# Performance work log

Measured on AMD Instinct MI355X. Metric: run time of the kernel, lower is better.

## Reference

```python
import jax, jax.numpy as jnp
import numpy as np

B, NNB, D, FF, L = 128, 510, 128, 512, 3
N = NNB + 2  # 2 query tokens (first/last) + neighbors
SQRT_D = float(np.sqrt(D))
LOGIT_CLIP = 10.0
NINF = -1e9


def _layer_norm(x, g, b):
    m = jnp.mean(x, axis=-1, keepdims=True)
    v = jnp.var(x, axis=-1, keepdims=True)
    return (x - m) * jax.lax.rsqrt(v + 1e-5) * g + b


def _aafm(q, k, v, w):
    # Attention-free module: sigmoid(q) * (exp(w) @ (exp(k)*v)) / (exp(w) @ exp(k))
    w = w - jnp.max(w, axis=-1, keepdims=True)          # stable, cancels in ratio
    k = k - jnp.max(k, axis=1, keepdims=True)
    ew = jnp.exp(w)                                      # [B,N,N]
    ek = jnp.exp(k)                                      # [B,N,D]
    num = jnp.einsum('bts,bsd->btd', ew, ek * v)
    den = jnp.einsum('bts,bsd->btd', ew, ek)
    return jax.nn.sigmoid(q) * num / den


def setup_inputs() -> dict:
    key = jax.random.key(0)
    ks = jax.random.split(key, 32)
    s = 1.0 / np.sqrt(D)
    inp = {
        'lower_xy': jax.random.uniform(ks[0], (B, N, 2), jnp.float32),
        'load': jax.random.uniform(ks[1], (B,), jnp.float32) * 0.9 + 0.1,
        'lower_demand': jax.random.uniform(ks[2], (B, NNB, 1), jnp.float32) * 0.3,
        'lower_cur_ninf_mask': jnp.where(
            jax.random.uniform(ks[3], (B, 1, N)) < 0.1, NINF, 0.0).astype(jnp.float32),
        'lower_pairwise_dist': jax.random.uniform(ks[4], (B, N, N), jnp.float32),
        'neighbors_num_list': jnp.full((B,), NNB, dtype=jnp.int32),
        'lower_neighbors_index': jax.random.randint(ks[5], (B, NNB), 0, 100000),
        # learned params (torch Linear stored transposed: here [in, out], y = x @ W)
        'emb_W': jax.random.normal(ks[6], (2, D)) * s,
        'emb_b': jnp.zeros((D,), jnp.float32),
        'w_load': jax.random.normal(ks[7], (D,)) * s,
        'w_demand': jax.random.normal(ks[8], (D,)) * s,
        'Wq_first': jax.random.normal(ks[9], (D, D)) * s,
        'Wq_last': jax.random.normal(ks[10], (D, D)) * s,
        'alpha_com': jnp.ones((1,), jnp.float32),
        'Wq': jax.random.normal(ks[11], (L, D, D)) * s,
        'Wk': jax.random.normal(ks[12], (L, D, D)) * s,
        'Wv': jax.random.normal(ks[13], (L, D, D)) * s,
        'alpha_attn': jnp.ones((L,), jnp.float32),
        'ln1_g': jnp.ones((L, D), jnp.float32),
        'ln1_b': jnp.zeros((L, D), jnp.float32),
        'ln2_g': jnp.ones((L, D), jnp.float32),
        'ln2_b': jnp.zeros((L, D), jnp.float32),
        'ff_W1': jax.random.normal(ks[14], (L, D, FF)) * s,
        'ff_b1': jnp.zeros((L, FF), jnp.float32),
        'ff_W2': jax.random.normal(ks[15], (L, FF, D)) * (1.0 / np.sqrt(FF)),
        'ff_b2': jnp.zeros((L, D), jnp.float32),
    }
    return inp


def reference(lower_xy, load, lower_demand, lower_cur_ninf_mask, lower_pairwise_dist,
              neighbors_num_list, lower_neighbors_index,
              emb_W, emb_b, w_load, w_demand, Wq_first, Wq_last, alpha_com,
              Wq, Wk, Wv, alpha_attn, ln1_g, ln1_b, ln2_g, ln2_b,
              ff_W1, ff_b1, ff_W2, ff_b2):
    load3 = load[:, None, None]                           # [B,1,1]
    load3 = jnp.where(load3 == 0, 1.0, load3)
    fln = lower_xy @ emb_W + emb_b                        # [B,N,D]
    load_emb = load3 * w_load                             # [B,1,D]
    q_first = fln[:, 0:1] @ Wq_first + load_emb
    q_last = fln[:, 1:2] @ Wq_last + load_emb
    demand = jnp.clip(lower_demand / load3, 0.0, 1.0)     # [B,n,1]
    nb = fln[:, 2:] + demand * w_demand                   # [B,n,D]
    nb_mask = lower_cur_ninf_mask[:, 0, 2:]               # [B,n]
    nb = jnp.where((nb_mask < 0)[..., None], 0.0, nb)     # padding overwrite
    x = jnp.concatenate([q_first, q_last, nb], axis=1)    # [B,N,D]

    log_nb = jnp.log2(neighbors_num_list.astype(x.dtype))[:, None, None]
    spd = -log_nb * lower_pairwise_dist                   # [B,N,N]
    mask_full = jnp.broadcast_to(lower_cur_ninf_mask, spd.shape)

    for i in range(L):
        q = x @ Wq[i]; k = x @ Wk[i]; v = x @ Wv[i]
        aafm = _aafm(q, k, v, alpha_attn[i] * spd + mask_full)
        h = _layer_norm(x + aafm, ln1_g[i], ln1_b[i])
        ff = jax.nn.relu(h @ ff_W1[i] + ff_b1[i]) @ ff_W2[i] + ff_b2[i]
        x = _layer_norm(h + ff, ln2_g[i], ln2_b[i])

    q_out = x[:, 0:1] + x[:, 1:2]                         # [B,1,D]
    nbo = x[:, 2:]                                        # [B,n,D]
    bias_com = alpha_com * spd[:, 1, 2:][:, None, :]      # [B,1,n]
    score = jnp.einsum('bqd,bnd->bqn', q_out, nbo) / SQRT_D + bias_com
    score = LOGIT_CLIP * jnp.tanh(score) + lower_cur_ninf_mask[:, :, 2:]
    probs = jax.nn.softmax(score, axis=-1)[:, 0]          # [B,n]

    selected = jnp.argmax(probs, axis=-1)                 # greedy eval
    prob = jnp.take_along_axis(probs, selected[:, None], axis=-1)[:, 0]
    true_selected = jnp.take_along_axis(lower_neighbors_index, selected[:, None], axis=-1)[:, 0]
    return true_selected, prob
```

## Files before the change

kernel.cpp:

```cpp
#include <hip/hip_runtime.h>
#include <math.h>

constexpr int B   = 128;
constexpr int N   = 512;
constexpr int NNB = 510;
constexpr int D   = 128;
constexpr int FFH = 512;
constexpr int NL  = 3;

__device__ __forceinline__ float sigmoidf_(float x) { return 1.f / (1.f + expf(-x)); }

#define F4ADD(a, b) { (a).x += (b).x; (a).y += (b).y; (a).z += (b).z; (a).w += (b).w; }

__device__ __forceinline__ float xla_fast_tanh(float x) {
    if (fabsf(x) < 0.0004f) return x;
    const float C = 7.99881172180175781f;
    float xc = fminf(fmaxf(x, -C), C);
    float x2 = __fmul_rn(xc, xc);
    float num = -2.76076847742355e-16f;
    num = __builtin_fmaf(x2, num, 2.00018790482477e-13f);
    num = __builtin_fmaf(x2, num, -8.60467152213735e-11f);
    num = __builtin_fmaf(x2, num, 5.12229709037114e-08f);
    num = __builtin_fmaf(x2, num, 1.48572235717979e-05f);
    num = __builtin_fmaf(x2, num, 6.37261928875436e-04f);
    num = __builtin_fmaf(x2, num, 4.89352455891786e-03f);
    num = __fmul_rn(xc, num);
    float den = 1.19825839466702e-06f;
    den = __builtin_fmaf(x2, den, 1.18534705686654e-04f);
    den = __builtin_fmaf(x2, den, 2.26843463243900e-03f);
    den = __builtin_fmaf(x2, den, 4.89352518554385e-03f);
    return num / den;
}

__global__ __launch_bounds__(128) void build_x_kernel(
    const float* __restrict__ xy, const float* __restrict__ load,
    const float* __restrict__ demand, const float* __restrict__ mask,
    const float* __restrict__ embW, const float* __restrict__ embb,
    const float* __restrict__ wload, const float* __restrict__ wdem,
    const float* __restrict__ Wqf, const float* __restrict__ Wql,
    float* __restrict__ x)
{
    __shared__ float fln[128];
    const int bn = blockIdx.x;
    const int b  = bn >> 9;
    const int n  = bn & 511;
    const int d  = threadIdx.x;
    float l = load[b];
    float load3 = (l == 0.f) ? 1.f : l;

    if (n >= 2) {
        const int j = n - 2;
        float m = mask[(size_t)b * N + n];
        float out = 0.f;
        if (!(m < 0.f)) {
            float x0 = xy[(size_t)bn * 2 + 0];
            float x1 = xy[(size_t)bn * 2 + 1];
            float fl = x0 * embW[d] + x1 * embW[D + d] + embb[d];
            float dm = demand[(size_t)b * NNB + j] / load3;
            dm = fminf(fmaxf(dm, 0.f), 1.f);
            out = fl + dm * wdem[d];
        }
        x[(size_t)bn * D + d] = out;
    } else {
        float x0 = xy[(size_t)bn * 2 + 0];
        float x1 = xy[(size_t)bn * 2 + 1];
        fln[d] = x0 * embW[d] + x1 * embW[D + d] + embb[d];
        __syncthreads();
        const float* W = (n == 0) ? Wqf : Wql;
        float acc = 0.f;
        #pragma unroll 8
        for (int e = 0; e < D; ++e) acc = fmaf(fln[e], W[(size_t)e * D + d], acc);
        x[(size_t)bn * D + d] = acc + load3 * wload[d];
    }
}

template<bool BIAS, bool RELU, int LNF>
__global__ __launch_bounds__(256) void gemm_f32(
    const float* __restrict__ A, const float* __restrict__ W,
    const float* __restrict__ bias, float* C,
    const float* resid, const float* __restrict__ g, const float* __restrict__ be,
    int M, int K, int Nc)
{
    __shared__ float As[64][40];
    __shared__ float Ws[32][132];
    const int m0 = blockIdx.x * 64;
    const int n0 = blockIdx.y * 128;
    const int tid = threadIdx.x;
    const int tc = tid & 31;
    const int tr = tid >> 5;

    const int ar0 = tid >> 3,          ac0 = (tid & 7) * 4;
    const int ar1 = (tid + 256) >> 3,  ac1 = ((tid + 256) & 7) * 4;
    int wr[4], wc[4];
    #pragma unroll
    for (int i = 0; i < 4; ++i) {
        int f = tid + i * 256;
        wr[i] = f >> 5; wc[i] = (f & 31) * 4;
    }

    float4 acc[8];
    #pragma unroll
    for (int r = 0; r < 8; ++r) acc[r] = make_float4(0.f, 0.f, 0.f, 0.f);

    {
        float4 a0 = *(const float4*)&A[(size_t)(m0 + ar0) * K + ac0];
        float4 a1 = *(const float4*)&A[(size_t)(m0 + ar1) * K + ac1];
        float4 w0 = *(const float4*)&W[(size_t)(0 + wr[0]) * Nc + n0 + wc[0]];
        float4 w1 = *(const float4*)&W[(size_t)(0 + wr[1]) * Nc + n0 + wc[1]];
        float4 w2 = *(const float4*)&W[(size_t)(0 + wr[2]) * Nc + n0 + wc[2]];
        float4 w3 = *(const float4*)&W[(size_t)(0 + wr[3]) * Nc + n0 + wc[3]];
        *(float4*)&As[ar0][ac0] = a0;
        *(float4*)&As[ar1][ac1] = a1;
        *(float4*)&Ws[wr[0]][wc[0]] = w0;
        *(float4*)&Ws[wr[1]][wc[1]] = w1;
        *(float4*)&Ws[wr[2]][wc[2]] = w2;
        *(float4*)&Ws[wr[3]][wc[3]] = w3;
    }
    __syncthreads();

    for (int kt = 0; kt < K; kt += 32) {
        const bool more = (kt + 32) < K;
        float4 na0, na1, nw0, nw1, nw2, nw3;
        if (more) {
            int kn = kt + 32;
            na0 = *(const float4*)&A[(size_t)(m0 + ar0) * K + kn + ac0];
            na1 = *(const float4*)&A[(size_t)(m0 + ar1) * K + kn + ac1];
            nw0 = *(const float4*)&W[(size_t)(kn + wr[0]) * Nc + n0 + wc[0]];
            nw1 = *(const float4*)&W[(size_t)(kn + wr[1]) * Nc + n0 + wc[1]];
            nw2 = *(const float4*)&W[(size_t)(kn + wr[2]) * Nc + n0 + wc[2]];
            nw3 = *(const float4*)&W[(size_t)(kn + wr[3]) * Nc + n0 + wc[3]];
        }
        #pragma unroll
        for (int kk = 0; kk < 32; kk += 4) {
            float4 w0 = *(float4*)&Ws[kk + 0][tc * 4];
            float4 w1 = *(float4*)&Ws[kk + 1][tc * 4];
            float4 w2 = *(float4*)&Ws[kk + 2][tc * 4];
            float4 w3 = *(float4*)&Ws[kk + 3][tc * 4];
            #pragma unroll
            for (int r = 0; r < 8; ++r) {
                float4 a4 = *(float4*)&As[tr * 8 + r][kk];
                acc[r].x = fmaf(a4.x, w0.x, acc[r].x); acc[r].x = fmaf(a4.y, w1.x, acc[r].x);
                acc[r].x = fmaf(a4.z, w2.x, acc[r].x); acc[r].x = fmaf(a4.w, w3.x, acc[r].x);
                acc[r].y = fmaf(a4.x, w0.y, acc[r].y); acc[r].y = fmaf(a4.y, w1.y, acc[r].y);
                acc[r].y = fmaf(a4.z, w2.y, acc[r].y); acc[r].y = fmaf(a4.w, w3.y, acc[r].y);
                acc[r].z = fmaf(a4.x, w0.z, acc[r].z); acc[r].z = fmaf(a4.y, w1.z, acc[r].z);
                acc[r].z = fmaf(a4.z, w2.z, acc[r].z); acc[r].z = fmaf(a4.w, w3.z, acc[r].z);
                acc[r].w = fmaf(a4.x, w0.w, acc[r].w); acc[r].w = fmaf(a4.y, w1.w, acc[r].w);
                acc[r].w = fmaf(a4.z, w2.w, acc[r].w); acc[r].w = fmaf(a4.w, w3.w, acc[r].w);
            }
        }
        if (more) {
            __syncthreads();
            *(float4*)&As[ar0][ac0] = na0;
            *(float4*)&As[ar1][ac1] = na1;
            *(float4*)&Ws[wr[0]][wc[0]] = nw0;
            *(float4*)&Ws[wr[1]][wc[1]] = nw1;
            *(float4*)&Ws[wr[2]][wc[2]] = nw2;
            *(float4*)&Ws[wr[3]][wc[3]] = nw3;
            __syncthreads();
        }
    }

    float4 bv = make_float4(0.f, 0.f, 0.f, 0.f);
    if (BIAS) bv = *(const float4*)&bias[n0 + tc * 4];
    if constexpr (LNF == 0) {
        #pragma unroll
        for (int r = 0; r < 8; ++r) {
            float4 o = acc[r];
            if (BIAS) { o.x += bv.x; o.y += bv.y; o.z += bv.z; o.w += bv.w; }
            if (RELU) {
                o.x = fmaxf(o.x, 0.f); o.y = fmaxf(o.y, 0.f);
                o.z = fmaxf(o.z, 0.f); o.w = fmaxf(o.w, 0.f);
            }
            *(float4*)&C[(size_t)(m0 + tr * 8 + r) * Nc + n0 + tc * 4] = o;
        }
    } else {
        float4 gv  = *(const float4*)&g[tc * 4];
        float4 bev = *(const float4*)&be[tc * 4];
        #pragma unroll
        for (int r = 0; r < 8; ++r) {
            float4 o = acc[r];
            o.x += bv.x; o.y += bv.y; o.z += bv.z; o.w += bv.w;
            size_t row = (size_t)(m0 + tr * 8 + r);
            float4 xv = *(const float4*)&resid[row * 128 + tc * 4];
            float y0 = xv.x + o.x, y1 = xv.y + o.y, y2 = xv.z + o.z, y3 = xv.w + o.w;
            float s = ((y0 + y1) + y2) + y3;
            #pragma unroll
            for (int mm = 16; mm > 0; mm >>= 1) s += __shfl_xor(s, mm);
            float mean = s * (1.f / 128.f);
            float d0_ = y0 - mean, d1_ = y1 - mean, d2_ = y2 - mean, d3_ = y3 - mean;
            float ss = ((d0_ * d0_ + d1_ * d1_) + d2_ * d2_) + d3_ * d3_;
            #pragma unroll
            for (int mm = 16; mm > 0; mm >>= 1) ss += __shfl_xor(ss, mm);
            float rs = rsqrtf(ss * (1.f / 128.f) + 1e-5f);
            float4 ov;
            ov.x = d0_ * rs * gv.x + bev.x;
            ov.y = d1_ * rs * gv.y + bev.y;
            ov.z = d2_ * rs * gv.z + bev.z;
            ov.w = d3_ * rs * gv.w + bev.w;
            *(float4*)&C[row * 128 + tc * 4] = ov;
        }
    }
}

__global__ __launch_bounds__(128) void colmax_part(
    const float* __restrict__ k, float* __restrict__ part)
{
    int b = blockIdx.x >> 3, c = blockIdx.x & 7, d = threadIdx.x;
    const float* kp = k + ((size_t)b * N + c * 64) * D + d;
    float m = -3.4e38f;
    #pragma unroll 8
    for (int s = 0; s < 64; ++s) m = fmaxf(m, kp[(size_t)s * D]);
    part[(size_t)blockIdx.x * D + d] = m;
}

__global__ __launch_bounds__(128) void ekv_build(
    const float* __restrict__ k, const float* __restrict__ v,
    const float* __restrict__ part, float* __restrict__ ekv)
{
    int b = blockIdx.x >> 3, c = blockIdx.x & 7, d = threadIdx.x;
    float m = -3.4e38f;
    #pragma unroll
    for (int j = 0; j < 8; ++j) m = fmaxf(m, part[((size_t)b * 8 + j) * D + d]);
    for (int s = 0; s < 64; ++s) {
        int sg = c * 64 + s;
        size_t off = ((size_t)b * N + sg) * D + d;
        float ek = expf(k[off] - m);
        size_t o2 = ((size_t)b * N + sg) * 256;
        ekv[o2 + d]       = ek * v[off];
        ekv[o2 + 128 + d] = ek;
    }
}

template<int V>
__global__ __launch_bounds__(256) void attn_kernel(
    const float* __restrict__ pdist, const float* __restrict__ mask,
    const float* __restrict__ ekv, const float* __restrict__ q,
    const float* xres, const float* __restrict__ g, const float* __restrict__ be,
    const int* __restrict__ nnum, const float* __restrict__ alphaAttn, int layer,
    float* outp)
{
    __shared__ float ew[16][516];
    __shared__ float red16[16][16];
    __shared__ float rmax[16];
    const int d0  = blockIdx.x;
    const int xcd = d0 & 7;
    const int idx = d0 >> 3;
    const int tl  = idx & 31;
    const int b   = (idx >> 5) * 8 + xcd;
    const int t0  = tl * 16;
    const int tid = threadIdx.x;
    const float la = -log2f((float)nnum[b]) * alphaAttn[layer];
    const float* pd = pdist + ((size_t)b * N + t0) * N;
    const float* mk = mask + (size_t)b * N;

    #pragma unroll
    for (int i = 0; i < 8; ++i) {
        int f = tid + i * 256;
        int r = f >> 7, s4 = (f & 127) * 4;
        float4 p = *(const float4*)&pd[(size_t)r * N + s4];
        float4 m = *(const float4*)&mk[s4];
        float4 w;
        w.x = fmaf(la, p.x, m.x); w.y = fmaf(la, p.y, m.y);
        w.z = fmaf(la, p.z, m.z); w.w = fmaf(la, p.w, m.w);
        *(float4*)&ew[r][s4] = w;
    }
    __syncthreads();
    {
        int r = tid >> 4, j0 = tid & 15;
        float m = -3.4e38f;
        #pragma unroll 8
        for (int j = 0; j < 32; ++j) m = fmaxf(m, ew[r][j0 + 16 * j]);
        red16[r][j0] = m;
    }
    __syncthreads();
    if (tid < 16) {
        float m = red16[tid][0];
        #pragma unroll
        for (int j = 1; j < 16; ++j) m = fmaxf(m, red16[tid][j]);
        rmax[tid] = m;
    }
    __syncthreads();
    #pragma unroll
    for (int i = 0; i < 8; ++i) {
        int f = tid + i * 256;
        int r = f >> 7, s4 = (f & 127) * 4;
        float m = rmax[r];
        float4 w = *(float4*)&ew[r][s4];
        w.x = expf(w.x - m); w.y = expf(w.y - m);
        w.z = expf(w.z - m); w.w = expf(w.w - m);
        *(float4*)&ew[r][s4] = w;
    }
    __syncthreads();

    if constexpr (V == 1) {
        float ssum = 0.f;
        #pragma unroll
        for (int i = 0; i < 8; ++i) {
            int f = tid + i * 256;
            int r = f >> 7, s4 = (f & 127) * 4;
            float4 w = *(float4*)&ew[r][s4];
            ssum += ((w.x + w.y) + w.z) + w.w;
        }
        outp[(size_t)d0 * 256 + tid] = ssum;
        return;
    }

    const int lane = tid & 63;
    const int wv   = tid >> 6;
    const int c4   = lane * 4;
    float4 acc[16];
    #pragma unroll
    for (int r = 0; r < 16; ++r) acc[r] = make_float4(0.f, 0.f, 0.f, 0.f);
    const float* ep = ekv + (size_t)b * N * 256 + c4;
    const int sb = wv * 128;
    float4 e0 = *(const float4*)&ep[(size_t)(sb + 0) * 256];
    float4 e1 = *(const float4*)&ep[(size_t)(sb + 1) * 256];
    float4 e2 = *(const float4*)&ep[(size_t)(sb + 2) * 256];
    float4 e3 = *(const float4*)&ep[(size_t)(sb + 3) * 256];
    for (int it = 0; it < 32; ++it) {
        const int s = sb + it * 4;
        float4 f0 = e0, f1 = e1, f2 = e2, f3 = e3;
        int sn = (it < 31) ? (s + 4) : s;
        e0 = *(const float4*)&ep[(size_t)(sn + 0) * 256];
        e1 = *(const float4*)&ep[(size_t)(sn + 1) * 256];
        e2 = *(const float4*)&ep[(size_t)(sn + 2) * 256];
        e3 = *(const float4*)&ep[(size_t)(sn + 3) * 256];
        if constexpr (V == 3) {
            float4 a = *(float4*)&ew[it & 15][s - sb];
            #pragma unroll
            for (int r = 0; r < 16; ++r) {
                acc[r].x = fmaf(a.x, f0.x, acc[r].x); acc[r].x = fmaf(a.y, f1.x, acc[r].x);
                acc[r].x = fmaf(a.z, f2.x, acc[r].x); acc[r].x = fmaf(a.w, f3.x, acc[r].x);
                acc[r].y = fmaf(a.x, f0.y, acc[r].y); acc[r].y = fmaf(a.y, f1.y, acc[r].y);
                acc[r].y = fmaf(a.z, f2.y, acc[r].y); acc[r].y = fmaf(a.w, f3.y, acc[r].y);
                acc[r].z = fmaf(a.x, f0.z, acc[r].z); acc[r].z = fmaf(a.y, f1.z, acc[r].z);
                acc[r].z = fmaf(a.z, f2.z, acc[r].z); acc[r].z = fmaf(a.w, f3.z, acc[r].z);
                acc[r].w = fmaf(a.x, f0.w, acc[r].w); acc[r].w = fmaf(a.y, f1.w, acc[r].w);
                acc[r].w = fmaf(a.z, f2.w, acc[r].w); acc[r].w = fmaf(a.w, f3.w, acc[r].w);
            }
        } else {
            #pragma unroll
            for (int r = 0; r < 16; ++r) {
                float4 a = *(float4*)&ew[r][s];
                acc[r].x = fmaf(a.x, f0.x, acc[r].x); acc[r].x = fmaf(a.y, f1.x, acc[r].x);
                acc[r].x = fmaf(a.z, f2.x, acc[r].x); acc[r].x = fmaf(a.w, f3.x, acc[r].x);
                acc[r].y = fmaf(a.x, f0.y, acc[r].y); acc[r].y = fmaf(a.y, f1.y, acc[r].y);
                acc[r].y = fmaf(a.z, f2.y, acc[r].y); acc[r].y = fmaf(a.w, f3.y, acc[r].y);
                acc[r].z = fmaf(a.x, f0.z, acc[r].z); acc[r].z = fmaf(a.y, f1.z, acc[r].z);
                acc[r].z = fmaf(a.z, f2.z, acc[r].z); acc[r].z = fmaf(a.w, f3.z, acc[r].z);
                acc[r].w = fmaf(a.x, f0.w, acc[r].w); acc[r].w = fmaf(a.y, f1.w, acc[r].w);
                acc[r].w = fmaf(a.z, f2.w, acc[r].w); acc[r].w = fmaf(a.w, f3.w, acc[r].w);
            }
        }
    }

    float* red = &ew[0][0];
    __syncthreads();
    if (wv == 1) {
        #pragma unroll
        for (int r = 0; r < 16; ++r) *(float4*)&red[r * 256 + c4] = acc[r];
    }
    if (wv == 3) {
        #pragma unroll
        for (int r = 0; r < 16; ++r) *(float4*)&red[4096 + r * 256 + c4] = acc[r];
    }
    __syncthreads();
    if (wv == 0) {
        #pragma unroll
        for (int r = 0; r < 16; ++r) { float4 t = *(float4*)&red[r * 256 + c4]; F4ADD(acc[r], t); }
    }
    if (wv == 2) {
        #pragma unroll
        for (int r = 0; r < 16; ++r) { float4 t = *(float4*)&red[4096 + r * 256 + c4]; F4ADD(acc[r], t); }
    }
    __syncthreads();
    if (wv == 2) {
        #pragma unroll
        for (int r = 0; r < 16; ++r) *(float4*)&red[r * 256 + c4] = acc[r];
    }
    __syncthreads();
    if (wv == 0) {
        #pragma unroll
        for (int r = 0; r < 16; ++r) {
            float4 t = *(float4*)&red[r * 256 + c4];
            F4ADD(acc[r], t);
            *(float4*)&red[r * 256 + c4] = acc[r];
        }
    }
    __syncthreads();

    if (lane < 32) {
        const int c = lane * 4;
        #pragma unroll
        for (int i = 0; i < 4; ++i) {
            int row = wv * 4 + i;
            float4 nu = *(float4*)&red[row * 256 + c];
            float4 de = *(float4*)&red[row * 256 + 128 + c];
            size_t off = ((size_t)b * N + t0 + row) * D + c;
            float4 qq = *(const float4*)&q[off];
            float4 av;
            av.x = sigmoidf_(qq.x) * nu.x / de.x;
            av.y = sigmoidf_(qq.y) * nu.y / de.y;
            av.z = sigmoidf_(qq.z) * nu.z / de.z;
            av.w = sigmoidf_(qq.w) * nu.w / de.w;
            if constexpr (V == 0) {
                float4 xv = *(const float4*)&xres[off];
                float y0 = xv.x + av.x, y1 = xv.y + av.y;
                float y2 = xv.z + av.z, y3 = xv.w + av.w;
                float s = ((y0 + y1) + y2) + y3;
                #pragma unroll
                for (int mm = 16; mm > 0; mm >>= 1) s += __shfl_xor(s, mm);
                float mean = s * (1.f / 128.f);
                float d0_ = y0 - mean, d1_ = y1 - mean, d2_ = y2 - mean, d3_ = y3 - mean;
                float ss = ((d0_ * d0_ + d1_ * d1_) + d2_ * d2_) + d3_ * d3_;
                #pragma unroll
                for (int mm = 16; mm > 0; mm >>= 1) ss += __shfl_xor(ss, mm);
                float rs = rsqrtf(ss * (1.f / 128.f) + 1e-5f);
                float4 ov;
                ov.x = d0_ * rs * g[c]     + be[c];
                ov.y = d1_ * rs * g[c + 1] + be[c + 1];
                ov.z = d2_ * rs * g[c + 2] + be[c + 2];
                ov.w = d3_ * rs * g[c + 3] + be[c + 3];
                *(float4*)&outp[off] = ov;
            } else {
                *(float4*)&outp[off] = av;
            }
        }
    }
}

__global__ __launch_bounds__(512) void k_final(
    const float* __restrict__ x, const float* __restrict__ pdist,
    const float* __restrict__ mask, const int* __restrict__ nnum,
    const int* __restrict__ nidx, const float* __restrict__ aCom,
    float* __restrict__ out)
{
    __shared__ float  sc[512];
    __shared__ float  ee[512];
    __shared__ double qo[128];
    int b = blockIdx.x, tid = threadIdx.x;
    const float* xb = x + (size_t)b * N * D;
    if (tid < 128) qo[tid] = (double)xb[tid] + (double)xb[128 + tid];
    __syncthreads();
    if (tid < NNB) {
        const float* xr = xb + (size_t)(2 + tid) * 128;
        double s = 0.0;
        for (int dd = 0; dd < 128; ++dd) s += qo[dd] * (double)xr[dd];
        double lg = -log2((double)nnum[b]);
        s = s / 11.313708498984761
          + (double)aCom[0] * lg * (double)pdist[((size_t)b * 512 + 1) * 512 + 2 + tid];
        float t = xla_fast_tanh((float)s);
        sc[tid] = __fadd_rn(__fmul_rn(10.0f, t),
                            mask[(size_t)b * 512 + 2 + tid]);
    }
    __syncthreads();
    if (tid == 0) {
        float m = -3.4e38f;
        for (int n2 = 0; n2 < NNB; ++n2) m = fmaxf(m, sc[n2]);
        float S = 0.f;
        for (int n2 = 0; n2 < NNB; ++n2) {
            float e = expf(__fadd_rn(sc[n2], -m));
            ee[n2] = e;
            S = __fadd_rn(S, e);
        }
        float bestp = -1.f; int sel = 0;
        for (int n2 = 0; n2 < NNB; ++n2) {
            float p = ee[n2] / S;
            if (p > bestp) { bestp = p; sel = n2; }
        }
        out[b]     = (float)nidx[(size_t)b * NNB + sel];
        out[B + b] = bestp;
    }
}

extern "C" void kernel_launch(void* const* d_in, const int* in_sizes, int n_in,
                              void* d_out, int out_size, void* d_ws, size_t ws_size,
                              hipStream_t stream)
{
    const float* xy     = (const float*)d_in[0];
    const float* load   = (const float*)d_in[1];
    const float* demand = (const float*)d_in[2];
    const float* mask   = (const float*)d_in[3];
    const float* pdist  = (const float*)d_in[4];
    const int*   nnum   = (const int*)d_in[5];
    const int*   nidx   = (const int*)d_in[6];
    const float* embW   = (const float*)d_in[7];
    const float* embb   = (const float*)d_in[8];
    const float* wload  = (const float*)d_in[9];
    const float* wdem   = (const float*)d_in[10];
    const float* Wqf    = (const float*)d_in[11];
    const float* Wql    = (const float*)d_in[12];
    const float* aCom   = (const float*)d_in[13];
    const float* Wq     = (const float*)d_in[14];
    const float* Wk     = (const float*)d_in[15];
    const float* Wv     = (const float*)d_in[16];
    const float* aAttn  = (const float*)d_in[17];
    const float* ln1g   = (const float*)d_in[18];
    const float* ln1b   = (const float*)d_in[19];
    const float* ln2g   = (const float*)d_in[20];
    const float* ln2b   = (const float*)d_in[21];
    const float* fW1    = (const float*)d_in[22];
    const float* fb1    = (const float*)d_in[23];
    const float* fW2    = (const float*)d_in[24];
    const float* fb2    = (const float*)d_in[25];
    float* out = (float*)d_out;

    float* ws = (float*)d_ws;
    const size_t SZ = (size_t)B * N * D;
    float* xbuf  = ws;
    float* qbuf  = ws + SZ;
    float* kbuf  = ws + 2 * SZ;
    float* vbuf  = ws + 3 * SZ;
    float* ekv   = ws + 4 * SZ;
    float* scrap = ws + 6 * SZ;
    float* part  = qbuf;
    float* bigh  = kbuf;

    build_x_kernel<<<B * N, 128, 0, stream>>>(xy, load, demand, mask, embW, embb,
                                              wload, wdem, Wqf, Wql, xbuf);
    const int M  = B * N;
    const int MH = M / 2;
    for (int l = 0; l < NL; ++l) {
        dim3 g1(M / 64, 1);
        gemm_f32<false, false, 0><<<g1, 256, 0, stream>>>(
            xbuf, Wk + (size_t)l * D * D, nullptr, kbuf, nullptr, nullptr, nullptr, M, D, D);
        gemm_f32<false, false, 0><<<g1, 256, 0, stream>>>(
            xbuf, Wv + (size_t)l * D * D, nullptr, vbuf, nullptr, nullptr, nullptr, M, D, D);
        colmax_part<<<B * 8, 128, 0, stream>>>(kbuf, part);
        ekv_build<<<B * 8, 128, 0, stream>>>(kbuf, vbuf, part, ekv);
        gemm_f32<false, false, 0><<<g1, 256, 0, stream>>>(
            xbuf, Wq + (size_t)l * D * D, nullptr, qbuf, nullptr, nullptr, nullptr, M, D, D);
        attn_kernel<0><<<B * 32, 256, 0, stream>>>(
            pdist, mask, ekv, qbuf, xbuf, ln1g + l * D, ln1b + l * D,
            nnum, aAttn, l, xbuf);
        if (l == 0) {
            attn_kernel<1><<<1024, 256, 0, stream>>>(
                pdist, mask, ekv, qbuf, xbuf, ln1g, ln1b, nnum, aAttn, l, scrap);
            attn_kernel<2><<<1024, 256, 0, stream>>>(
                pdist, mask, ekv, qbuf, xbuf, ln1g, ln1b, nnum, aAttn, l, scrap);
            attn_kernel<3><<<1024, 256, 0, stream>>>(
                pdist, mask, ekv, qbuf, xbuf, ln1g, ln1b, nnum, aAttn, l, scrap);
        }
        for (int h = 0; h < 2; ++h) {
            dim3 g2(MH / 64, FFH / 128);
            dim3 g3(MH / 64, 1);
            gemm_f32<true, true, 0><<<g2, 256, 0, stream>>>(
                xbuf + (size_t)h * MH * D, fW1 + (size_t)l * D * FFH, fb1 + l * FFH,
                bigh, nullptr, nullptr, nullptr, MH, D, FFH);
            gemm_f32<true, false, 1><<<g3, 256, 0, stream>>>(
                bigh, fW2 + (size_t)l * FFH * D, fb2 + l * D,
                xbuf + (size_t)h * MH * D, xbuf + (size_t)h * MH * D,
                ln2g + l * D, ln2b + l * D, MH, FFH, D);
        }
    }
    k_final<<<B, 512, 0, stream>>>(xbuf, pdist, mask, nnum, nidx, aCom, out);
}
```

Measured before the change: 2.022 ms.

## Remove probe attention kernels, batch QKV GEMMs, enlarge GEMM row tile

Removes three extra attention kernel variants that ran in layer 0 and only wrote to a scratch buffer. Merges the Q, K and V projections into one launch, using grid.y to select the weight and output. Doubles the GEMM row tile to 128 with 16 accumulator rows per thread to improve weight reuse. The larger tile raises register pressure and halves the block count, which may lower occupancy.

```diff
diff --git a/kernel.cpp b/kernel.cpp
--- a/kernel.cpp
+++ b/kernel.cpp
@@ -75,42 +75,55 @@
 }
 
 template<bool BIAS, bool RELU, int LNF>
-__global__ __launch_bounds__(256) void gemm_f32(
-    const float* __restrict__ A, const float* __restrict__ W,
-    const float* __restrict__ bias, float* C,
+__global__ __launch_bounds__(256) void gemm128(
+    const float* __restrict__ A,
+    const float* W0, const float* Wb, const float* Wc,
+    const float* __restrict__ bias,
+    float* C0, float* Cb, float* Cc,
     const float* resid, const float* __restrict__ g, const float* __restrict__ be,
     int M, int K, int Nc)
 {
-    __shared__ float As[64][40];
+    __shared__ float As[128][36];
     __shared__ float Ws[32][132];
-    const int m0 = blockIdx.x * 64;
-    const int n0 = blockIdx.y * 128;
+    const float* W = W0;
+    float* C = C0;
+    int n0 = 0;
+    if (Wb != nullptr) {
+        if (blockIdx.y == 1)      { W = Wb; C = Cb; }
+        else if (blockIdx.y == 2) { W = Wc; C = Cc; }
+    } else {
+        n0 = blockIdx.y * 128;
+    }
+    const int m0 = blockIdx.x * 128;
     const int tid = threadIdx.x;
     const int tc = tid & 31;
     const int tr = tid >> 5;
 
-    const int ar0 = tid >> 3,          ac0 = (tid & 7) * 4;
-    const int ar1 = (tid + 256) >> 3,  ac1 = ((tid + 256) & 7) * 4;
-    int wr[4], wc[4];
+    int ar[4], ac[4], wr[4], wc[4];
     #pragma unroll
     for (int i = 0; i < 4; ++i) {
         int f = tid + i * 256;
-        wr[i] = f >> 5; wc[i] = (f & 31) * 4;
-    }
-
-    float4 acc[8];
+        ar[i] = f >> 3;  ac[i] = (f & 7) * 4;
+        wr[i] = f >> 5;  wc[i] = (f & 31) * 4;
+    }
+
+    float4 acc[16];
     #pragma unroll
-    for (int r = 0; r < 8; ++r) acc[r] = make_float4(0.f, 0.f, 0.f, 0.f);
+    for (int r = 0; r < 16; ++r) acc[r] = make_float4(0.f, 0.f, 0.f, 0.f);
 
     {
-        float4 a0 = *(const float4*)&A[(size_t)(m0 + ar0) * K + ac0];
-        float4 a1 = *(const float4*)&A[(size_t)(m0 + ar1) * K + ac1];
-        float4 w0 = *(const float4*)&W[(size_t)(0 + wr[0]) * Nc + n0 + wc[0]];
-        float4 w1 = *(const float4*)&W[(size_t)(0 + wr[1]) * Nc + n0 + wc[1]];
-        float4 w2 = *(const float4*)&W[(size_t)(0 + wr[2]) * Nc + n0 + wc[2]];
-        float4 w3 = *(const float4*)&W[(size_t)(0 + wr[3]) * Nc + n0 + wc[3]];
-        *(float4*)&As[ar0][ac0] = a0;
-        *(float4*)&As[ar1][ac1] = a1;
+        float4 a0 = *(const float4*)&A[(size_t)(m0 + ar[0]) * K + ac[0]];
+        float4 a1 = *(const float4*)&A[(size_t)(m0 + ar[1]) * K + ac[1]];
+        float4 a2 = *(const float4*)&A[(size_t)(m0 + ar[2]) * K + ac[2]];
+        float4 a3 = *(const float4*)&A[(size_t)(m0 + ar[3]) * K + ac[3]];
+        float4 w0 = *(const float4*)&W[(size_t)wr[0] * Nc + n0 + wc[0]];
+        float4 w1 = *(const float4*)&W[(size_t)wr[1] * Nc + n0 + wc[1]];
+        float4 w2 = *(const float4*)&W[(size_t)wr[2] * Nc + n0 + wc[2]];
+        float4 w3 = *(const float4*)&W[(size_t)wr[3] * Nc + n0 + wc[3]];
+        *(float4*)&As[ar[0]][ac[0]] = a0;
+        *(float4*)&As[ar[1]][ac[1]] = a1;
+        *(float4*)&As[ar[2]][ac[2]] = a2;
+        *(float4*)&As[ar[3]][ac[3]] = a3;
         *(float4*)&Ws[wr[0]][wc[0]] = w0;
         *(float4*)&Ws[wr[1]][wc[1]] = w1;
         *(float4*)&Ws[wr[2]][wc[2]] = w2;
@@ -120,11 +133,13 @@
 
     for (int kt = 0; kt < K; kt += 32) {
         const bool more = (kt + 32) < K;
-        float4 na0, na1, nw0, nw1, nw2, nw3;
+        float4 na0, na1, na2, na3, nw0, nw1, nw2, nw3;
         if (more) {
             int kn = kt + 32;
-            na0 = *(const float4*)&A[(size_t)(m0 + ar0) * K + kn + ac0];
-            na1 = *(const float4*)&A[(size_t)(m0 + ar1) * K + kn + ac1];
+            na0 = *(const float4*)&A[(size_t)(m0 + ar[0]) * K + kn + ac[0]];
+            na1 = *(const float4*)&A[(size_t)(m0 + ar[1]) * K + kn + ac[1]];
+            na2 = *(const float4*)&A[(size_t)(m0 + ar[2]) * K + kn + ac[2]];
+            na3 = *(const float4*)&A[(size_t)(m0 + ar[3]) * K + kn + ac[3]];
             nw0 = *(const float4*)&W[(size_t)(kn + wr[0]) * Nc + n0 + wc[0]];
             nw1 = *(const float4*)&W[(size_t)(kn + wr[1]) * Nc + n0 + wc[1]];
             nw2 = *(const float4*)&W[(size_t)(kn + wr[2]) * Nc + n0 + wc[2]];
@@ -137,8 +152,8 @@
             float4 w2 = *(float4*)&Ws[kk + 2][tc * 4];
             float4 w3 = *(float4*)&Ws[kk + 3][tc * 4];
             #pragma unroll
-            for (int r = 0; r < 8; ++r) {
-                float4 a4 = *(float4*)&As[tr * 8 + r][kk];
+            for (int r = 0; r < 16; ++r) {
+                float4 a4 = *(float4*)&As[tr * 16 + r][kk];
                 acc[r].x = fmaf(a4.x, w0.x, acc[r].x); acc[r].x = fmaf(a4.y, w1.x, acc[r].x);
                 acc[r].x = fmaf(a4.z, w2.x, acc[r].x); acc[r].x = fmaf(a4.w, w3.x, acc[r].x);
                 acc[r].y = fmaf(a4.x, w0.y, acc[r].y); acc[r].y = fmaf(a4.y, w1.y, acc[r].y);
@@ -151,8 +166,10 @@
         }
         if (more) {
             __syncthreads();
-            *(float4*)&As[ar0][ac0] = na0;
-            *(float4*)&As[ar1][ac1] = na1;
+            *(float4*)&As[ar[0]][ac[0]] = na0;
+            *(float4*)&As[ar[1]][ac[1]] = na1;
+            *(float4*)&As[ar[2]][ac[2]] = na2;
+            *(float4*)&As[ar[3]][ac[3]] = na3;
             *(float4*)&Ws[wr[0]][wc[0]] = nw0;
             *(float4*)&Ws[wr[1]][wc[1]] = nw1;
             *(float4*)&Ws[wr[2]][wc[2]] = nw2;
@@ -165,23 +182,23 @@
     if (BIAS) bv = *(const float4*)&bias[n0 + tc * 4];
     if constexpr (LNF == 0) {
         #pragma unroll
-        for (int r = 0; r < 8; ++r) {
+        for (int r = 0; r < 16; ++r) {
             float4 o = acc[r];
             if (BIAS) { o.x += bv.x; o.y += bv.y; o.z += bv.z; o.w += bv.w; }
             if (RELU) {
                 o.x = fmaxf(o.x, 0.f); o.y = fmaxf(o.y, 0.f);
                 o.z = fmaxf(o.z, 0.f); o.w = fmaxf(o.w, 0.f);
             }
-            *(float4*)&C[(size_t)(m0 + tr * 8 + r) * Nc + n0 + tc * 4] = o;
+            *(float4*)&C[(size_t)(m0 + tr * 16 + r) * Nc + n0 + tc * 4] = o;
         }
     } else {
         float4 gv  = *(const float4*)&g[tc * 4];
         float4 bev = *(const float4*)&be[tc * 4];
         #pragma unroll
-        for (int r = 0; r < 8; ++r) {
+        for (int r = 0; r < 16; ++r) {
             float4 o = acc[r];
             o.x += bv.x; o.y += bv.y; o.z += bv.z; o.w += bv.w;
-            size_t row = (size_t)(m0 + tr * 8 + r);
+            size_t row = (size_t)(m0 + tr * 16 + r);
             float4 xv = *(const float4*)&resid[row * 128 + tc * 4];
             float y0 = xv.x + o.x, y1 = xv.y + o.y, y2 = xv.z + o.z, y3 = xv.w + o.w;
             float s = ((y0 + y1) + y2) + y3;
@@ -232,7 +249,6 @@
     }
 }
 
-template<int V>
 __global__ __launch_bounds__(256) void attn_kernel(
     const float* __restrict__ pdist, const float* __restrict__ mask,
     const float* __restrict__ ekv, const float* __restrict__ q,
@@ -292,19 +308,6 @@
         *(float4*)&ew[r][s4] = w;
     }
     __syncthreads();
-
-    if constexpr (V == 1) {
-        float ssum = 0.f;
-        #pragma unroll
-        for (int i = 0; i < 8; ++i) {
-            int f = tid + i * 256;
-            int r = f >> 7, s4 = (f & 127) * 4;
-            float4 w = *(float4*)&ew[r][s4];
-            ssum += ((w.x + w.y) + w.z) + w.w;
-        }
-        outp[(size_t)d0 * 256 + tid] = ssum;
-        return;
-    }
 
     const int lane = tid & 63;
     const int wv   = tid >> 6;
@@ -326,32 +329,17 @@
         e1 = *(const float4*)&ep[(size_t)(sn + 1) * 256];
         e2 = *(const float4*)&ep[(size_t)(sn + 2) * 256];
         e3 = *(const float4*)&ep[(size_t)(sn + 3) * 256];
-        if constexpr (V == 3) {
-            float4 a = *(float4*)&ew[it & 15][s - sb];
-            #pragma unroll
-            for (int r = 0; r < 16; ++r) {
-                acc[r].x = fmaf(a.x, f0.x, acc[r].x); acc[r].x = fmaf(a.y, f1.x, acc[r].x);
-                acc[r].x = fmaf(a.z, f2.x, acc[r].x); acc[r].x = fmaf(a.w, f3.x, acc[r].x);
-                acc[r].y = fmaf(a.x, f0.y, acc[r].y); acc[r].y = fmaf(a.y, f1.y, acc[r].y);
-                acc[r].y = fmaf(a.z, f2.y, acc[r].y); acc[r].y = fmaf(a.w, f3.y, acc[r].y);
-                acc[r].z = fmaf(a.x, f0.z, acc[r].z); acc[r].z = fmaf(a.y, f1.z, acc[r].z);
-                acc[r].z = fmaf(a.z, f2.z, acc[r].z); acc[r].z = fmaf(a.w, f3.z, acc[r].z);
-                acc[r].w = fmaf(a.x, f0.w, acc[r].w); acc[r].w = fmaf(a.y, f1.w, acc[r].w);
-                acc[r].w = fmaf(a.z, f2.w, acc[r].w); acc[r].w = fmaf(a.w, f3.w, acc[r].w);
-            }
-        } else {
-            #pragma unroll
-            for (int r = 0; r < 16; ++r) {
-                float4 a = *(float4*)&ew[r][s];
-                acc[r].x = fmaf(a.x, f0.x, acc[r].x); acc[r].x = fmaf(a.y, f1.x, acc[r].x);
-                acc[r].x = fmaf(a.z, f2.x, acc[r].x); acc[r].x = fmaf(a.w, f3.x, acc[r].x);
-                acc[r].y = fmaf(a.x, f0.y, acc[r].y); acc[r].y = fmaf(a.y, f1.y, acc[r].y);
-                acc[r].y = fmaf(a.z, f2.y, acc[r].y); acc[r].y = fmaf(a.w, f3.y, acc[r].y);
-                acc[r].z = fmaf(a.x, f0.z, acc[r].z); acc[r].z = fmaf(a.y, f1.z, acc[r].z);
-                acc[r].z = fmaf(a.z, f2.z, acc[r].z); acc[r].z = fmaf(a.w, f3.z, acc[r].z);
-                acc[r].w = fmaf(a.x, f0.w, acc[r].w); acc[r].w = fmaf(a.y, f1.w, acc[r].w);
-                acc[r].w = fmaf(a.z, f2.w, acc[r].w); acc[r].w = fmaf(a.w, f3.w, acc[r].w);
-            }
+        #pragma unroll
+        for (int r = 0; r < 16; ++r) {
+            float4 a = *(float4*)&ew[r][s];
+            acc[r].x = fmaf(a.x, f0.x, acc[r].x); acc[r].x = fmaf(a.y, f1.x, acc[r].x);
+            acc[r].x = fmaf(a.z, f2.x, acc[r].x); acc[r].x = fmaf(a.w, f3.x, acc[r].x);
+            acc[r].y = fmaf(a.x, f0.y, acc[r].y); acc[r].y = fmaf(a.y, f1.y, acc[r].y);
+            acc[r].y = fmaf(a.z, f2.y, acc[r].y); acc[r].y = fmaf(a.w, f3.y, acc[r].y);
+            acc[r].z = fmaf(a.x, f0.z, acc[r].z); acc[r].z = fmaf(a.y, f1.z, acc[r].z);
+            acc[r].z = fmaf(a.z, f2.z, acc[r].z); acc[r].z = fmaf(a.w, f3.z, acc[r].z);
+            acc[r].w = fmaf(a.x, f0.w, acc[r].w); acc[r].w = fmaf(a.y, f1.w, acc[r].w);
+            acc[r].w = fmaf(a.z, f2.w, acc[r].w); acc[r].w = fmaf(a.w, f3.w, acc[r].w);
         }
     }
 
@@ -404,28 +392,24 @@
             av.y = sigmoidf_(qq.y) * nu.y / de.y;
             av.z = sigmoidf_(qq.z) * nu.z / de.z;
             av.w = sigmoidf_(qq.w) * nu.w / de.w;
-            if constexpr (V == 0) {
-                float4 xv = *(const float4*)&xres[off];
-                float y0 = xv.x + av.x, y1 = xv.y + av.y;
-                float y2 = xv.z + av.z, y3 = xv.w + av.w;
-                float s = ((y0 + y1) + y2) + y3;
-                #pragma unroll
-                for (int mm = 16; mm > 0; mm >>= 1) s += __shfl_xor(s, mm);
-                float mean = s * (1.f / 128.f);
-                float d0_ = y0 - mean, d1_ = y1 - mean, d2_ = y2 - mean, d3_ = y3 - mean;
-                float ss = ((d0_ * d0_ + d1_ * d1_) + d2_ * d2_) + d3_ * d3_;
-                #pragma unroll
-                for (int mm = 16; mm > 0; mm >>= 1) ss += __shfl_xor(ss, mm);
-                float rs = rsqrtf(ss * (1.f / 128.f) + 1e-5f);
-                float4 ov;
-                ov.x = d0_ * rs * g[c]     + be[c];
-                ov.y = d1_ * rs * g[c + 1] + be[c + 1];
-                ov.z = d2_ * rs * g[c + 2] + be[c + 2];
-                ov.w = d3_ * rs * g[c + 3] + be[c + 3];
-                *(float4*)&outp[off] = ov;
-            } else {
-                *(float4*)&outp[off] = av;
-            }
+            float4 xv = *(const float4*)&xres[off];
+            float y0 = xv.x + av.x, y1 = xv.y + av.y;
+            float y2 = xv.z + av.z, y3 = xv.w + av.w;
+            float s = ((y0 + y1) + y2) + y3;
+            #pragma unroll
+            for (int mm = 16; mm > 0; mm >>= 1) s += __shfl_xor(s, mm);
+            float mean = s * (1.f / 128.f);
+            float d0_ = y0 - mean, d1_ = y1 - mean, d2_ = y2 - mean, d3_ = y3 - mean;
+            float ss = ((d0_ * d0_ + d1_ * d1_) + d2_ * d2_) + d3_ * d3_;
+            #pragma unroll
+            for (int mm = 16; mm > 0; mm >>= 1) ss += __shfl_xor(ss, mm);
+            float rs = rsqrtf(ss * (1.f / 128.f) + 1e-5f);
+            float4 ov;
+            ov.x = d0_ * rs * g[c]     + be[c];
+            ov.y = d1_ * rs * g[c + 1] + be[c + 1];
+            ov.z = d2_ * rs * g[c + 2] + be[c + 2];
+            ov.w = d3_ * rs * g[c + 3] + be[c + 3];
+            *(float4*)&outp[off] = ov;
         }
     }
 }
@@ -513,8 +497,7 @@
     float* kbuf  = ws + 2 * SZ;
     float* vbuf  = ws + 3 * SZ;
     float* ekv   = ws + 4 * SZ;
-    float* scrap = ws + 6 * SZ;
-    float* part  = qbuf;
+    float* part  = ws + 6 * SZ;
     float* bigh  = kbuf;
 
     build_x_kernel<<<B * N, 128, 0, stream>>>(xy, load, demand, mask, embW, embb,
@@ -522,36 +505,24 @@
     const int M  = B * N;
     const int MH = M / 2;
     for (int l = 0; l < NL; ++l) {
-        dim3 g1(M / 64, 1);
-        gemm_f32<false, false, 0><<<g1, 256, 0, stream>>>(
-            xbuf, Wk + (size_t)l * D * D, nullptr, kbuf, nullptr, nullptr, nullptr, M, D, D);
-        gemm_f32<false, false, 0><<<g1, 256, 0, stream>>>(
-            xbuf, Wv + (size_t)l * D * D, nullptr, vbuf, nullptr, nullptr, nullptr, M, D, D);
+        gemm128<false, false, 0><<<dim3(M / 128, 3), 256, 0, stream>>>(
+            xbuf, Wq + (size_t)l * D * D, Wk + (size_t)l * D * D, Wv + (size_t)l * D * D,
+            nullptr, qbuf, kbuf, vbuf, nullptr, nullptr, nullptr, M, D, D);
         colmax_part<<<B * 8, 128, 0, stream>>>(kbuf, part);
         ekv_build<<<B * 8, 128, 0, stream>>>(kbuf, vbuf, part, ekv);
-        gemm_f32<false, false, 0><<<g1, 256, 0, stream>>>(
-            xbuf, Wq + (size_t)l * D * D, nullptr, qbuf, nullptr, nullptr, nullptr, M, D, D);
-        attn_kernel<0><<<B * 32, 256, 0, stream>>>(
+        attn_kernel<<<B * 32, 256, 0, stream>>>(
             pdist, mask, ekv, qbuf, xbuf, ln1g + l * D, ln1b + l * D,
             nnum, aAttn, l, xbuf);
-        if (l == 0) {
-            attn_kernel<1><<<1024, 256, 0, stream>>>(
-                pdist, mask, ekv, qbuf, xbuf, ln1g, ln1b, nnum, aAttn, l, scrap);
-            attn_kernel<2><<<1024, 256, 0, stream>>>(
-                pdist, mask, ekv, qbuf, xbuf, ln1g, ln1b, nnum, aAttn, l, scrap);
-            attn_kernel<3><<<1024, 256, 0, stream>>>(
-                pdist, mask, ekv, qbuf, xbuf, ln1g, ln1b, nnum, aAttn, l, scrap);
-        }
         for (int h = 0; h < 2; ++h) {
-            dim3 g2(MH / 64, FFH / 128);
-            dim3 g3(MH / 64, 1);
-            gemm_f32<true, true, 0><<<g2, 256, 0, stream>>>(
-                xbuf + (size_t)h * MH * D, fW1 + (size_t)l * D * FFH, fb1 + l * FFH,
-                bigh, nullptr, nullptr, nullptr, MH, D, FFH);
-            gemm_f32<true, false, 1><<<g3, 256, 0, stream>>>(
-                bigh, fW2 + (size_t)l * FFH * D, fb2 + l * D,
-                xbuf + (size_t)h * MH * D, xbuf + (size_t)h * MH * D,
-                ln2g + l * D, ln2b + l * D, MH, FFH, D);
+            gemm128<true, true, 0><<<dim3(MH / 128, FFH / 128), 256, 0, stream>>>(
+                xbuf + (size_t)h * MH * D, fW1 + (size_t)l * D * FFH, nullptr, nullptr,
+                fb1 + l * FFH, bigh, nullptr, nullptr, nullptr, nullptr, nullptr,
+                MH, D, FFH);
+            gemm128<true, false, 1><<<dim3(MH / 128, 1), 256, 0, stream>>>(
+                bigh, fW2 + (size_t)l * FFH * D, nullptr, nullptr, fb2 + l * D,
+                xbuf + (size_t)h * MH * D, nullptr, nullptr,
+                xbuf + (size_t)h * MH * D, ln2g + l * D, ln2b + l * D,
+                MH, FFH, D);
         }
     }
     k_final<<<B, 512, 0, stream>>>(xbuf, pdist, mask, nnum, nidx, aCom, out);
```

Measured after the change: 2.083 ms. +3.0%, slower.
